# Performance work log

Measured on AMD Instinct MI355X. Metric: run time of the kernel, lower is better.

Reference implementation:

```python
import jax, jax.numpy as jnp
import numpy as np

N = 20000          # nodes
E = 320000         # edges (avg degree 16)
D_IN, D1, D2, D_OUT = 256, 512, 256, 64
EPS = 1e-5


def _glorot(key, shape):
    lim = (6.0 / (shape[0] + shape[1])) ** 0.5
    return jax.random.uniform(key, shape, jnp.float32, -lim, lim)


def setup_inputs() -> dict:
    key = jax.random.key(0)
    ks = jax.random.split(key, 8)
    x = jax.random.normal(ks[0], (N, D_IN), jnp.float32)
    edge_index = jax.random.randint(ks[1], (2, E), 0, N, dtype=jnp.int64)
    return {
        "x": x,
        "edge_index": edge_index,
        # SAGEConv 1 (SoftmaxAggregation temperature t1 over inp_dim channels)
        "t1": jnp.ones((1, D_IN), jnp.float32),
        "Wl1": _glorot(ks[2], (D_IN, D1)), "bl1": jnp.zeros((D1,), jnp.float32),
        "Wr1": _glorot(ks[3], (D_IN, D1)),
        "g1": jnp.ones((D1,), jnp.float32), "beta1": jnp.zeros((D1,), jnp.float32),
        # SAGEConv 2
        "t2": jnp.ones((1, D1), jnp.float32),
        "Wl2": _glorot(ks[4], (D1, D2)), "bl2": jnp.zeros((D2,), jnp.float32),
        "Wr2": _glorot(ks[5], (D1, D2)),
        "g2": jnp.ones((D2,), jnp.float32), "beta2": jnp.zeros((D2,), jnp.float32),
        # final linear + LayerNorm
        "Wf": _glorot(ks[6], (D2, D_OUT)), "bf": jnp.zeros((D_OUT,), jnp.float32),
        "gx": jnp.ones((D_OUT,), jnp.float32), "betax": jnp.zeros((D_OUT,), jnp.float32),
    }


def _sage_softmax(x, src, dst, t, Wl, bl, Wr, n):
    """SAGEConv with learnable per-channel SoftmaxAggregation."""
    m = x[src]                                              # [E, C] gathered messages
    a = m * t                                               # scaled logits
    amax = jax.ops.segment_max(a, dst, num_segments=n)      # [N, C]
    e = jnp.exp(a - amax[dst])
    denom = jax.ops.segment_sum(e, dst, num_segments=n)     # [N, C]
    w = e / denom[dst]                                      # segment softmax weights
    agg = jax.ops.segment_sum(m * w, dst, num_segments=n)   # weighted neighbor sum
    return agg @ Wl + bl + x @ Wr


def _graph_ln(x, g, b):
    # PyG LayerNorm mode='graph', batch=None: normalize over ALL nodes & channels
    mu = x.mean()
    std = jnp.sqrt(((x - mu) ** 2).mean())
    return (x - mu) / (std + EPS) * g + b


def _ln(x, g, b):
    mu = x.mean(-1, keepdims=True)
    var = ((x - mu) ** 2).mean(-1, keepdims=True)
    return (x - mu) / jnp.sqrt(var + EPS) * g + b


def reference(x, edge_index, t1, Wl1, bl1, Wr1, g1, beta1,
              t2, Wl2, bl2, Wr2, g2, beta2, Wf, bf, gx, betax):
    src, dst = edge_index[0], edge_index[1]
    h = _sage_softmax(x, src, dst, t1, Wl1, bl1, Wr1, N)
    h = jax.nn.relu(_graph_ln(h, g1, beta1))
    h = _sage_softmax(h, src, dst, t2, Wl2, bl2, Wr2, N)
    h = jax.nn.relu(_graph_ln(h, g2, beta2))
    p = h.mean(0, keepdims=True)                            # global_mean_pool, batch=None -> [1, 256]
    out = _ln(p @ Wf + bf, gx, betax)
    return jax.nn.relu(out)
```

## Files before the change

kernel.cpp:

```cpp
#include <hip/hip_runtime.h>
#include <math.h>

#define NODES 20000
#define EDGES 320000
#define EPSV  1e-5f
#define LOG2E 1.4426950408889634f

typedef short bf16x8 __attribute__((ext_vector_type(8)));
typedef float f32x4  __attribute__((ext_vector_type(4)));

__device__ __forceinline__ unsigned short f2bf(float f) {
    unsigned int u = __float_as_uint(f);
    u = (u + 0x7fffu + ((u >> 16) & 1u)) >> 16;
    return (unsigned short)u;
}
__device__ __forceinline__ float bf2f(unsigned short h) {
    return __uint_as_float(((unsigned int)h) << 16);
}

__global__ void k_count(const int* __restrict__ dst, int* __restrict__ counts) {
    int e = blockIdx.x * blockDim.x + threadIdx.x;
    if (e < EDGES) atomicAdd(&counts[dst[e]], 1);
}

__global__ void k_scan(const int* __restrict__ counts, int* __restrict__ offs) {
    __shared__ int ssum[256];
    int t = threadIdx.x;
    const int chunk = (NODES + 255) / 256;
    int b = t * chunk, e = b + chunk;
    if (b > NODES) b = NODES;
    if (e > NODES) e = NODES;
    int s = 0;
    for (int i = b; i < e; i++) s += counts[i];
    ssum[t] = s;
    __syncthreads();
    if (t == 0) {
        int run = 0;
        for (int i = 0; i < 256; i++) { int v = ssum[i]; ssum[i] = run; run += v; }
        offs[NODES] = run;
    }
    __syncthreads();
    int run = ssum[t];
    for (int i = b; i < e; i++) { offs[i] = run; run += counts[i]; }
}

__global__ void k_scatter(const int* __restrict__ src, const int* __restrict__ dst,
                          const int* __restrict__ offs, int* __restrict__ cursor,
                          int* __restrict__ csr_src) {
    int e = blockIdx.x * blockDim.x + threadIdx.x;
    if (e < EDGES) {
        int d = dst[e];
        int pos = atomicAdd(&cursor[d], 1);
        csr_src[offs[d] + pos] = src[e];
    }
}

__global__ void k_cast(const float* __restrict__ in, unsigned short* __restrict__ out) {
    int i = (blockIdx.x * blockDim.x + threadIdx.x) * 4;
    float4 v = *(const float4*)(in + i);
    out[i + 0] = f2bf(v.x); out[i + 1] = f2bf(v.y);
    out[i + 2] = f2bf(v.z); out[i + 3] = f2bf(v.w);
}

__global__ void k_transpose_all(const float* __restrict__ Wl1, const float* __restrict__ Wr1,
                                const float* __restrict__ Wl2, const float* __restrict__ Wr2,
                                unsigned short* __restrict__ o1l, unsigned short* __restrict__ o1r,
                                unsigned short* __restrict__ o2l, unsigned short* __restrict__ o2r) {
    __shared__ float tile[32][33];
    int z = blockIdx.z;
    const float* W = (z == 0) ? Wl1 : (z == 1) ? Wr1 : (z == 2) ? Wl2 : Wr2;
    unsigned short* Wt = (z == 0) ? o1l : (z == 1) ? o1r : (z == 2) ? o2l : o2r;
    int K = (z < 2) ? 256 : 512, N = (z < 2) ? 512 : 256;
    int nb = N / 32;
    int n0 = (blockIdx.x % nb) * 32, k0 = (blockIdx.x / nb) * 32;
    int tx = threadIdx.x, ty = threadIdx.y;
#pragma unroll
    for (int j = 0; j < 4; j++)
        tile[ty + j * 8][tx] = W[(size_t)(k0 + ty + j * 8) * N + n0 + tx];
    __syncthreads();
#pragma unroll
    for (int j = 0; j < 4; j++)
        Wt[(size_t)(n0 + ty + j * 8) * K + k0 + tx] = f2bf(tile[tx][ty + j * 8]);
}

template <int C>
__global__ void k_agg(const unsigned short* __restrict__ xb, const float* __restrict__ tt,
                      const int* __restrict__ offs, const int* __restrict__ csr,
                      unsigned short* __restrict__ out) {
    constexpr int VPL = C / 64;
    typedef unsigned short usv __attribute__((ext_vector_type(VPL)));
    int wave = (int)((blockIdx.x * (unsigned)blockDim.x + threadIdx.x) >> 6);
    int lane = threadIdx.x & 63;
    if (wave >= NODES) return;
    int beg = offs[wave], end = offs[wave + 1];
    int cb = lane * VPL;
    float tl[VPL], l[VPL], s[VPL];
#pragma unroll
    for (int i = 0; i < VPL; i++) { tl[i] = tt[cb + i] * LOG2E; l[i] = 0.f; s[i] = 0.f; }
    int k = beg;
    for (; k + 1 < end; k += 2) {
        int sn0 = csr[k], sn1 = csr[k + 1];
        usv v0 = *(const usv*)(xb + (size_t)sn0 * C + cb);
        usv v1 = *(const usv*)(xb + (size_t)sn1 * C + cb);
#pragma unroll
        for (int i = 0; i < VPL; i++) {
            float x0 = bf2f(v0[i]);
            float x1 = bf2f(v1[i]);
            float p0 = __builtin_amdgcn_exp2f(x0 * tl[i]);
            float p1 = __builtin_amdgcn_exp2f(x1 * tl[i]);
            l[i] += p0;
            s[i] = fmaf(p0, x0, s[i]);
            l[i] += p1;
            s[i] = fmaf(p1, x1, s[i]);
        }
    }
    if (k < end) {
        int sn = csr[k];
        usv v = *(const usv*)(xb + (size_t)sn * C + cb);
#pragma unroll
        for (int i = 0; i < VPL; i++) {
            float xv = bf2f(v[i]);
            float p = __builtin_amdgcn_exp2f(xv * tl[i]);
            l[i] += p;
            s[i] = fmaf(p, xv, s[i]);
        }
    }
    bool has = end > beg;
    usv o;
#pragma unroll
    for (int i = 0; i < VPL; i++) o[i] = f2bf(has ? s[i] / l[i] : 0.f);
    *(usv*)(out + (size_t)wave * C + cb) = o;
}

template <int K, int NT>
__global__ __launch_bounds__(256) void k_gemm_mfma(
    const unsigned short* __restrict__ A1, const unsigned short* __restrict__ B1t,
    const unsigned short* __restrict__ A2, const unsigned short* __restrict__ B2t,
    const float* __restrict__ bias, unsigned short* __restrict__ Co, int M,
    float* __restrict__ stat) {
    __shared__ short As[128 * 40];
    __shared__ short Bs[128 * 40];
    __shared__ float rs[256], rq[256];

    int t = threadIdx.x;
    int m0 = blockIdx.x * 128, n0 = blockIdx.y * 128;
    int wv = t >> 6, lane = t & 63;
    int wm = wv & 1, wn = wv >> 1;
    int lm = lane & 15, quad = lane >> 4;
    int sr = t >> 2;
    int sk = (t & 3) * 8;

    f32x4 acc[4][4] = {};

    for (int ph = 0; ph < 2; ph++) {
        const unsigned short* __restrict__ A  = ph ? A2 : A1;
        const unsigned short* __restrict__ Bt = ph ? B2t : B1t;
        for (int k0 = 0; k0 < K; k0 += 32) {
#pragma unroll
            for (int it = 0; it < 2; it++) {
                int r = sr + it * 64;
                int mm = m0 + r;
                bf16x8 va;
#pragma unroll
                for (int j = 0; j < 8; j++) va[j] = 0;
                if (mm < M) va = *(const bf16x8*)(A + (size_t)mm * K + k0 + sk);
                *(bf16x8*)&As[r * 40 + sk] = va;
                bf16x8 vb = *(const bf16x8*)(Bt + (size_t)(n0 + r) * K + k0 + sk);
                *(bf16x8*)&Bs[r * 40 + sk] = vb;
            }
            __syncthreads();
            bf16x8 af[4], bfr[4];
#pragma unroll
            for (int i = 0; i < 4; i++) {
                af[i]  = *(const bf16x8*)&As[(wm * 64 + i * 16 + lm) * 40 + quad * 8];
                bfr[i] = *(const bf16x8*)&Bs[(wn * 64 + i * 16 + lm) * 40 + quad * 8];
            }
#pragma unroll
            for (int mi = 0; mi < 4; mi++)
#pragma unroll
                for (int nj = 0; nj < 4; nj++)
                    acc[mi][nj] = __builtin_amdgcn_mfma_f32_16x16x32_bf16(
                        af[mi], bfr[nj], acc[mi][nj], 0, 0, 0);
            __syncthreads();
        }
    }

    float sum = 0.f, ss = 0.f;
#pragma unroll
    for (int mi = 0; mi < 4; mi++) {
        int rb = m0 + wm * 64 + mi * 16 + quad * 4;
#pragma unroll
        for (int nj = 0; nj < 4; nj++) {
            int col = n0 + wn * 64 + nj * 16 + lm;
            float bb = bias[col];
#pragma unroll
            for (int rg = 0; rg < 4; rg++) {
                int row = rb + rg;
                if (row < M) {
                    float y = acc[mi][nj][rg] + bb;
                    Co[(size_t)row * NT + col] = f2bf(y);
                    sum += y; ss += y * y;
                }
            }
        }
    }
    rs[t] = sum; rq[t] = ss;
    __syncthreads();
    for (int o = 128; o > 0; o >>= 1) {
        if (t < o) { rs[t] += rs[t + o]; rq[t] += rq[t + o]; }
        __syncthreads();
    }
    if (t == 0) { atomicAdd(&stat[0], rs[0]); atomicAdd(&stat[1], rq[0]); }
}

template <int C>
__global__ void k_ln_relu_b(unsigned short* __restrict__ h, int n,
                            const float* __restrict__ st,
                            const float* __restrict__ g, const float* __restrict__ b) {
    typedef unsigned short us8 __attribute__((ext_vector_type(8)));
    float mu = st[0] / (float)n;
    float var = st[1] / (float)n - mu * mu;
    var = var < 0.f ? 0.f : var;
    float inv = 1.0f / (sqrtf(var) + EPSV);
    int i8 = (blockIdx.x * blockDim.x + threadIdx.x) * 8;
    if (i8 >= n) return;
    int c = i8 & (C - 1);
    us8 v = *(const us8*)(h + i8);
    us8 o;
#pragma unroll
    for (int j = 0; j < 8; j++) {
        float y = (bf2f(v[j]) - mu) * inv * g[c + j] + b[c + j];
        o[j] = f2bf(fmaxf(y, 0.f));
    }
    *(us8*)(h + i8) = o;
}

__global__ void k_ln_colsum(const unsigned short* __restrict__ h, int n,
                            const float* __restrict__ st,
                            const float* __restrict__ g, const float* __restrict__ b,
                            float* __restrict__ colsum) {
    float mu = st[0] / (float)n;
    float var = st[1] / (float)n - mu * mu;
    var = var < 0.f ? 0.f : var;
    float inv = 1.0f / (sqrtf(var) + EPSV);
    int t = threadIdx.x;
    float gv = g[t], bv = b[t];
    float local = 0.f;
    int stride = gridDim.x * blockDim.x;
    for (int i = blockIdx.x * blockDim.x + t; i < n; i += stride) {
        float y = (bf2f(h[i]) - mu) * inv * gv + bv;
        local += fmaxf(y, 0.f);
    }
    atomicAdd(&colsum[t], local);
}

__global__ void k_final(const float* __restrict__ colsum, const float* __restrict__ Wf,
                        const float* __restrict__ bf, const float* __restrict__ gx,
                        const float* __restrict__ bx, float* __restrict__ out) {
    __shared__ float p[256];
    int t = threadIdx.x;
    p[t] = colsum[t] * (1.0f / (float)NODES);
    __syncthreads();
    if (t < 64) {
        float acc = bf[t];
        for (int c = 0; c < 256; c++) acc = fmaf(p[c], Wf[c * 64 + t], acc);
        float sum = acc;
        for (int o = 32; o > 0; o >>= 1) sum += __shfl_xor(sum, o);
        float mu = sum * (1.0f / 64.0f);
        float d = acc - mu;
        float vs = d * d;
        for (int o = 32; o > 0; o >>= 1) vs += __shfl_xor(vs, o);
        float var = vs * (1.0f / 64.0f);
        float y = d * rsqrtf(var + EPSV) * gx[t] + bx[t];
        out[t] = fmaxf(y, 0.f);
    }
}

extern "C" void kernel_launch(void* const* d_in, const int* in_sizes, int n_in,
                              void* d_out, int out_size, void* d_ws, size_t ws_size,
                              hipStream_t stream) {
    const float* x   = (const float*)d_in[0];
    const int*   ei  = (const int*)d_in[1];
    const float* t1  = (const float*)d_in[2];
    const float* Wl1 = (const float*)d_in[3];
    const float* bl1 = (const float*)d_in[4];
    const float* Wr1 = (const float*)d_in[5];
    const float* g1  = (const float*)d_in[6];
    const float* be1 = (const float*)d_in[7];
    const float* t2  = (const float*)d_in[8];
    const float* Wl2 = (const float*)d_in[9];
    const float* bl2 = (const float*)d_in[10];
    const float* Wr2 = (const float*)d_in[11];
    const float* g2  = (const float*)d_in[12];
    const float* be2 = (const float*)d_in[13];
    const float* Wf  = (const float*)d_in[14];
    const float* bf  = (const float*)d_in[15];
    const float* gx  = (const float*)d_in[16];
    const float* bx  = (const float*)d_in[17];
    float* out = (float*)d_out;

    char* ws = (char*)d_ws;
    size_t off = 0;
    auto alloc = [&](size_t bytes) { size_t o = off; off = (off + bytes + 511) & ~511ull; return o; };
    size_t o_counts = alloc((size_t)NODES * 4);
    size_t o_cursor = alloc((size_t)NODES * 4);
    size_t o_acc    = alloc(4 * 4);
    size_t o_colsum = alloc(256 * 4);
    size_t zero_bytes = off;
    size_t o_offs = alloc((size_t)(NODES + 1) * 4);
    size_t o_csrc = alloc((size_t)EDGES * 4);
    size_t o_w1l  = alloc((size_t)512 * 256 * 2);
    size_t o_w1r  = alloc((size_t)512 * 256 * 2);
    size_t o_w2l  = alloc((size_t)256 * 512 * 2);
    size_t o_w2r  = alloc((size_t)256 * 512 * 2);
    size_t o_bufX = alloc((size_t)NODES * 256 * 2);
    size_t o_agg  = alloc((size_t)NODES * 512 * 2);
    size_t o_h1   = alloc((size_t)NODES * 512 * 2);

    int*   counts = (int*)(ws + o_counts);
    int*   cursor = (int*)(ws + o_cursor);
    float* acc    = (float*)(ws + o_acc);
    float* colsum = (float*)(ws + o_colsum);
    int*   offs   = (int*)(ws + o_offs);
    int*   csrc   = (int*)(ws + o_csrc);
    unsigned short* w1lt = (unsigned short*)(ws + o_w1l);
    unsigned short* w1rt = (unsigned short*)(ws + o_w1r);
    unsigned short* w2lt = (unsigned short*)(ws + o_w2l);
    unsigned short* w2rt = (unsigned short*)(ws + o_w2r);
    unsigned short* xb   = (unsigned short*)(ws + o_bufX);
    unsigned short* h2p  = (unsigned short*)(ws + o_bufX);
    unsigned short* aggb = (unsigned short*)(ws + o_agg);
    unsigned short* h1   = (unsigned short*)(ws + o_h1);

    const int* src = ei;
    const int* dst = ei + EDGES;

    hipMemsetAsync(ws, 0, zero_bytes, stream);

    k_count<<<(EDGES + 255) / 256, 256, 0, stream>>>(dst, counts);
    k_scan<<<1, 256, 0, stream>>>(counts, offs);
    k_scatter<<<(EDGES + 255) / 256, 256, 0, stream>>>(src, dst, offs, cursor, csrc);
    k_cast<<<NODES * 256 / 4 / 256, 256, 0, stream>>>(x, xb);
    k_transpose_all<<<dim3(128, 1, 4), dim3(32, 8), 0, stream>>>(
        Wl1, Wr1, Wl2, Wr2, w1lt, w1rt, w2lt, w2rt);

    k_agg<256><<<(NODES + 3) / 4, 256, 0, stream>>>(xb, t1, offs, csrc, aggb);
    k_gemm_mfma<256, 512><<<dim3((NODES + 127) / 128, 4), 256, 0, stream>>>(
        aggb, w1lt, xb, w1rt, bl1, h1, NODES, acc);
    k_ln_relu_b<512><<<NODES * 512 / 8 / 256, 256, 0, stream>>>(h1, NODES * 512, acc, g1, be1);

    k_agg<512><<<(NODES + 3) / 4, 256, 0, stream>>>(h1, t2, offs, csrc, aggb);
    k_gemm_mfma<512, 256><<<dim3((NODES + 127) / 128, 2), 256, 0, stream>>>(
        aggb, w2lt, h1, w2rt, bl2, h2p, NODES, acc + 2);
    k_ln_colsum<<<1024, 256, 0, stream>>>(h2p, NODES * 256, acc + 2, g2, be2, colsum);

    k_final<<<1, 256, 0, stream>>>(colsum, Wf, bf, gx, bx, out);
}
```

Baseline: 372.1 us.

## Use direct global-to-LDS loads in GEMM and unroll packed aggregation

The GEMM tile staging now uses global_load_lds to copy A and B tiles straight into LDS, dropping the register round-trip and the row-bound check. Buffers are padded to a multiple of 128 rows so reads past the last node stay inside the allocation. The LDS row stride drops from 40 to 32, which removes the padding and may add bank conflicts on the fragment reads. The aggregation kernel gains a configurable edge unroll (4 for C=256, 2 for C=512) and works on packed float2 values to issue more gathers in flight and use fewer VALU ops. The padded rows are never zeroed, so garbage rows enter the GEMM and its epilogue has to mask them to keep the statistics correct.

```diff
diff --git a/kernel.cpp b/kernel.cpp
--- a/kernel.cpp
+++ b/kernel.cpp
@@ -2,12 +2,14 @@
 #include <math.h>
 
 #define NODES 20000
+#define MPAD  20096
 #define EDGES 320000
 #define EPSV  1e-5f
 #define LOG2E 1.4426950408889634f
 
 typedef short bf16x8 __attribute__((ext_vector_type(8)));
 typedef float f32x4  __attribute__((ext_vector_type(4)));
+typedef float f2     __attribute__((ext_vector_type(2)));
 
 __device__ __forceinline__ unsigned short f2bf(float f) {
     unsigned int u = __float_as_uint(f);
@@ -16,6 +18,12 @@
 }
 __device__ __forceinline__ float bf2f(unsigned short h) {
     return __uint_as_float(((unsigned int)h) << 16);
+}
+
+__device__ __forceinline__ void load_lds16(const unsigned short* g, unsigned short* l) {
+    __builtin_amdgcn_global_load_lds(
+        (const __attribute__((address_space(1))) unsigned int*)g,
+        (__attribute__((address_space(3))) unsigned int*)l, 16, 0, 0);
 }
 
 __global__ void k_count(const int* __restrict__ dst, int* __restrict__ counts) {
@@ -83,52 +91,75 @@
         Wt[(size_t)(n0 + ty + j * 8) * K + k0 + tx] = f2bf(tile[tx][ty + j * 8]);
 }
 
-template <int C>
+template <int C, int UNR>
 __global__ void k_agg(const unsigned short* __restrict__ xb, const float* __restrict__ tt,
                       const int* __restrict__ offs, const int* __restrict__ csr,
                       unsigned short* __restrict__ out) {
     constexpr int VPL = C / 64;
+    constexpr int W = VPL / 2;
+    typedef unsigned int uv __attribute__((ext_vector_type(W)));
     typedef unsigned short usv __attribute__((ext_vector_type(VPL)));
     int wave = (int)((blockIdx.x * (unsigned)blockDim.x + threadIdx.x) >> 6);
     int lane = threadIdx.x & 63;
     if (wave >= NODES) return;
     int beg = offs[wave], end = offs[wave + 1];
     int cb = lane * VPL;
-    float tl[VPL], l[VPL], s[VPL];
-#pragma unroll
-    for (int i = 0; i < VPL; i++) { tl[i] = tt[cb + i] * LOG2E; l[i] = 0.f; s[i] = 0.f; }
+    f2 tl[W], l[W], s[W];
+#pragma unroll
+    for (int i = 0; i < W; i++) {
+        tl[i][0] = tt[cb + 2 * i] * LOG2E;
+        tl[i][1] = tt[cb + 2 * i + 1] * LOG2E;
+        l[i][0] = 0.f; l[i][1] = 0.f;
+        s[i][0] = 0.f; s[i][1] = 0.f;
+    }
     int k = beg;
-    for (; k + 1 < end; k += 2) {
-        int sn0 = csr[k], sn1 = csr[k + 1];
-        usv v0 = *(const usv*)(xb + (size_t)sn0 * C + cb);
-        usv v1 = *(const usv*)(xb + (size_t)sn1 * C + cb);
-#pragma unroll
-        for (int i = 0; i < VPL; i++) {
-            float x0 = bf2f(v0[i]);
-            float x1 = bf2f(v1[i]);
-            float p0 = __builtin_amdgcn_exp2f(x0 * tl[i]);
-            float p1 = __builtin_amdgcn_exp2f(x1 * tl[i]);
-            l[i] += p0;
-            s[i] = fmaf(p0, x0, s[i]);
-            l[i] += p1;
-            s[i] = fmaf(p1, x1, s[i]);
+    for (; k + UNR <= end; k += UNR) {
+        uv v[UNR];
+#pragma unroll
+        for (int u = 0; u < UNR; u++) {
+            int sn = csr[k + u];
+            v[u] = *(const uv*)(xb + (size_t)sn * C + cb);
         }
-    }
-    if (k < end) {
+#pragma unroll
+        for (int u = 0; u < UNR; u++)
+#pragma unroll
+            for (int i = 0; i < W; i++) {
+                unsigned wd = v[u][i];
+                f2 xv;
+                xv[0] = __uint_as_float(wd << 16);
+                xv[1] = __uint_as_float(wd & 0xffff0000u);
+                f2 a = xv * tl[i];
+                f2 p;
+                p[0] = __builtin_amdgcn_exp2f(a[0]);
+                p[1] = __builtin_amdgcn_exp2f(a[1]);
+                l[i] += p;
+                s[i] = __builtin_elementwise_fma(p, xv, s[i]);
+            }
+    }
+    for (; k < end; k++) {
         int sn = csr[k];
-        usv v = *(const usv*)(xb + (size_t)sn * C + cb);
-#pragma unroll
-        for (int i = 0; i < VPL; i++) {
-            float xv = bf2f(v[i]);
-            float p = __builtin_amdgcn_exp2f(xv * tl[i]);
+        uv vv = *(const uv*)(xb + (size_t)sn * C + cb);
+#pragma unroll
+        for (int i = 0; i < W; i++) {
+            unsigned wd = vv[i];
+            f2 xv;
+            xv[0] = __uint_as_float(wd << 16);
+            xv[1] = __uint_as_float(wd & 0xffff0000u);
+            f2 a = xv * tl[i];
+            f2 p;
+            p[0] = __builtin_amdgcn_exp2f(a[0]);
+            p[1] = __builtin_amdgcn_exp2f(a[1]);
             l[i] += p;
-            s[i] = fmaf(p, xv, s[i]);
+            s[i] = __builtin_elementwise_fma(p, xv, s[i]);
         }
     }
     bool has = end > beg;
     usv o;
 #pragma unroll
-    for (int i = 0; i < VPL; i++) o[i] = f2bf(has ? s[i] / l[i] : 0.f);
+    for (int i = 0; i < W; i++) {
+        o[2 * i]     = f2bf(has ? s[i][0] / l[i][0] : 0.f);
+        o[2 * i + 1] = f2bf(has ? s[i][1] / l[i][1] : 0.f);
+    }
     *(usv*)(out + (size_t)wave * C + cb) = o;
 }
 
@@ -138,8 +169,8 @@
     const unsigned short* __restrict__ A2, const unsigned short* __restrict__ B2t,
     const float* __restrict__ bias, unsigned short* __restrict__ Co, int M,
     float* __restrict__ stat) {
-    __shared__ short As[128 * 40];
-    __shared__ short Bs[128 * 40];
+    __shared__ short As[128 * 32];
+    __shared__ short Bs[128 * 32];
     __shared__ float rs[256], rq[256];
 
     int t = threadIdx.x;
@@ -148,7 +179,7 @@
     int wm = wv & 1, wn = wv >> 1;
     int lm = lane & 15, quad = lane >> 4;
     int sr = t >> 2;
-    int sk = (t & 3) * 8;
+    int sc8 = (t & 3) * 8;
 
     f32x4 acc[4][4] = {};
 
@@ -158,22 +189,17 @@
         for (int k0 = 0; k0 < K; k0 += 32) {
 #pragma unroll
             for (int it = 0; it < 2; it++) {
-                int r = sr + it * 64;
-                int mm = m0 + r;
-                bf16x8 va;
-#pragma unroll
-                for (int j = 0; j < 8; j++) va[j] = 0;
-                if (mm < M) va = *(const bf16x8*)(A + (size_t)mm * K + k0 + sk);
-                *(bf16x8*)&As[r * 40 + sk] = va;
-                bf16x8 vb = *(const bf16x8*)(Bt + (size_t)(n0 + r) * K + k0 + sk);
-                *(bf16x8*)&Bs[r * 40 + sk] = vb;
+                load_lds16(A  + (size_t)(m0 + it * 64 + sr) * K + k0 + sc8,
+                           (unsigned short*)&As[it * 2048 + wv * 512]);
+                load_lds16(Bt + (size_t)(n0 + it * 64 + sr) * K + k0 + sc8,
+                           (unsigned short*)&Bs[it * 2048 + wv * 512]);
             }
             __syncthreads();
             bf16x8 af[4], bfr[4];
 #pragma unroll
             for (int i = 0; i < 4; i++) {
-                af[i]  = *(const bf16x8*)&As[(wm * 64 + i * 16 + lm) * 40 + quad * 8];
-                bfr[i] = *(const bf16x8*)&Bs[(wn * 64 + i * 16 + lm) * 40 + quad * 8];
+                af[i]  = *(const bf16x8*)&As[(wm * 64 + i * 16 + lm) * 32 + quad * 8];
+                bfr[i] = *(const bf16x8*)&Bs[(wn * 64 + i * 16 + lm) * 32 + quad * 8];
             }
 #pragma unroll
             for (int mi = 0; mi < 4; mi++)
@@ -313,9 +339,9 @@
     size_t o_w1r  = alloc((size_t)512 * 256 * 2);
     size_t o_w2l  = alloc((size_t)256 * 512 * 2);
     size_t o_w2r  = alloc((size_t)256 * 512 * 2);
-    size_t o_bufX = alloc((size_t)NODES * 256 * 2);
-    size_t o_agg  = alloc((size_t)NODES * 512 * 2);
-    size_t o_h1   = alloc((size_t)NODES * 512 * 2);
+    size_t o_bufX = alloc((size_t)MPAD * 256 * 2);
+    size_t o_agg  = alloc((size_t)MPAD * 512 * 2);
+    size_t o_h1   = alloc((size_t)MPAD * 512 * 2);
 
     int*   counts = (int*)(ws + o_counts);
     int*   cursor = (int*)(ws + o_cursor);
@@ -344,13 +370,13 @@
     k_transpose_all<<<dim3(128, 1, 4), dim3(32, 8), 0, stream>>>(
         Wl1, Wr1, Wl2, Wr2, w1lt, w1rt, w2lt, w2rt);
 
-    k_agg<256><<<(NODES + 3) / 4, 256, 0, stream>>>(xb, t1, offs, csrc, aggb);
-    k_gemm_mfma<256, 512><<<dim3((NODES + 127) / 128, 4), 256, 0, stream>>>(
+    k_agg<256, 4><<<(NODES + 3) / 4, 256, 0, stream>>>(xb, t1, offs, csrc, aggb);
+    k_gemm_mfma<256, 512><<<dim3(MPAD / 128, 4), 256, 0, stream>>>(
         aggb, w1lt, xb, w1rt, bl1, h1, NODES, acc);
     k_ln_relu_b<512><<<NODES * 512 / 8 / 256, 256, 0, stream>>>(h1, NODES * 512, acc, g1, be1);
 
-    k_agg<512><<<(NODES + 3) / 4, 256, 0, stream>>>(h1, t2, offs, csrc, aggb);
-    k_gemm_mfma<512, 256><<<dim3((NODES + 127) / 128, 2), 256, 0, stream>>>(
+    k_agg<512, 2><<<(NODES + 3) / 4, 256, 0, stream>>>(h1, t2, offs, csrc, aggb);
+    k_gemm_mfma<512, 256><<<dim3(MPAD / 128, 2), 256, 0, stream>>>(
         aggb, w2lt, h1, w2rt, bl2, h2p, NODES, acc + 2);
     k_ln_colsum<<<1024, 256, 0, stream>>>(h2p, NODES * 256, acc + 2, g2, be2, colsum);
 
```

Result: faster. 359.3 us (-3.4%).
